# Kernel optimization log

Measured on AMD Instinct MI355X. Metric: run time of the kernel, lower is better.

## Reference

```python
import jax, jax.numpy as jnp
import numpy as np

D_MODEL = 1024
N_HEADS = 16
HEAD_DIM = D_MODEL // N_HEADS
D_FF = 4096
B, T = 2, 2048
LN_EPS = 1e-5


def setup_inputs() -> dict:
    key = jax.random.key(0)
    ks = jax.random.split(key, 12)
    s = 0.02
    return {
        "x": jax.random.normal(ks[0], (B, T, D_MODEL), jnp.float32),
        "ln1_g": jnp.ones((D_MODEL,), jnp.float32),
        "ln1_b": jnp.zeros((D_MODEL,), jnp.float32),
        "w_qkv": jax.random.normal(ks[1], (D_MODEL, 3 * D_MODEL), jnp.float32) * s,
        "b_qkv": jnp.zeros((3 * D_MODEL,), jnp.float32),
        "w_out": jax.random.normal(ks[2], (D_MODEL, D_MODEL), jnp.float32) * s,
        "b_out": jnp.zeros((D_MODEL,), jnp.float32),
        "ln2_g": jnp.ones((D_MODEL,), jnp.float32),
        "ln2_b": jnp.zeros((D_MODEL,), jnp.float32),
        "w_ff1": jax.random.normal(ks[3], (D_MODEL, D_FF), jnp.float32) * s,
        "b_ff1": jnp.zeros((D_FF,), jnp.float32),
        "w_ff2": jax.random.normal(ks[4], (D_FF, D_MODEL), jnp.float32) * s,
        "b_ff2": jnp.zeros((D_MODEL,), jnp.float32),
    }


def _layernorm(x, g, b):
    mu = jnp.mean(x, axis=-1, keepdims=True)
    var = jnp.mean(jnp.square(x - mu), axis=-1, keepdims=True)
    return (x - mu) * jax.lax.rsqrt(var + LN_EPS) * g + b


def _attention(h, w_qkv, b_qkv, w_out, b_out):
    Bx, Tx, C = h.shape
    qkv = h @ w_qkv + b_qkv  # [B,T,3C]
    q, k, v = jnp.split(qkv, 3, axis=-1)
    # [B,H,T,Dh]
    q = q.reshape(Bx, Tx, N_HEADS, HEAD_DIM).transpose(0, 2, 1, 3)
    k = k.reshape(Bx, Tx, N_HEADS, HEAD_DIM).transpose(0, 2, 1, 3)
    v = v.reshape(Bx, Tx, N_HEADS, HEAD_DIM).transpose(0, 2, 1, 3)
    scale = 1.0 / np.sqrt(HEAD_DIM).astype(np.float32)
    scores = jnp.einsum("bhqd,bhkd->bhqk", q, k) * scale
    causal = jnp.tril(jnp.ones((Tx, Tx), bool))
    scores = jnp.where(causal[None, None], scores, -jnp.inf)
    attn = jax.nn.softmax(scores, axis=-1)
    out = jnp.einsum("bhqk,bhkd->bhqd", attn, v)
    out = out.transpose(0, 2, 1, 3).reshape(Bx, Tx, C)
    return out @ w_out + b_out


def reference(x, ln1_g, ln1_b, w_qkv, b_qkv, w_out, b_out,
              ln2_g, ln2_b, w_ff1, b_ff1, w_ff2, b_ff2):
    h = _layernorm(x, ln1_g, ln1_b)
    x = x + _attention(h, w_qkv, b_qkv, w_out, b_out)
    h2 = _layernorm(x, ln2_g, ln2_b)
    ff = jax.nn.relu(h2 @ w_ff1 + b_ff1) @ w_ff2 + b_ff2
    return x + ff
```

## Files before the change

### kernel.cpp

```cpp
#include <hip/hip_runtime.h>


typedef unsigned short u16;
typedef __attribute__((ext_vector_type(8))) short     bf16x8;
typedef __attribute__((ext_vector_type(4))) float     f32x4;
typedef __attribute__((ext_vector_type(8))) unsigned short u16x8;
typedef __attribute__((ext_vector_type(4))) unsigned short u16x4;

__device__ __forceinline__ u16 f2bf(float f) {
    unsigned u = __builtin_bit_cast(unsigned, f);
    unsigned r = (u + 0x7fffu + ((u >> 16) & 1u)) >> 16;
    return (u16)r;
}
__device__ __forceinline__ float bf2f(u16 h) {
    unsigned u = ((unsigned)h) << 16;
    return __builtin_bit_cast(float, u);
}
__device__ __forceinline__ f32x4 mfma16(bf16x8 a, bf16x8 b, f32x4 c) {
    return __builtin_amdgcn_mfma_f32_16x16x32_bf16(a, b, c, 0, 0, 0);
}
__device__ __forceinline__ void gl_lds16(const u16* g, u16* l) {
    __builtin_amdgcn_global_load_lds((const __attribute__((address_space(1))) void*)g,
                                     (__attribute__((address_space(3))) void*)l, 16, 0, 0);
}

__global__ __launch_bounds__(256) void wconv_kernel(const float* __restrict__ in, u16* __restrict__ out,
                                                    int R, int C) {
    __shared__ float t[32][33];
    const int tx = threadIdx.x, ty = threadIdx.y;
    const int c0 = blockIdx.x * 32, r0 = blockIdx.y * 32;
#pragma unroll
    for (int i = 0; i < 4; ++i)
        t[ty + 8 * i][tx] = in[(size_t)(r0 + ty + 8 * i) * C + c0 + tx];
    __syncthreads();
#pragma unroll
    for (int i = 0; i < 4; ++i)
        out[(size_t)(c0 + ty + 8 * i) * R + r0 + tx] = f2bf(t[tx][ty + 8 * i]);
}

__global__ __launch_bounds__(256) void ln_kernel(const float* __restrict__ x, const float* __restrict__ g,
                                                 const float* __restrict__ b, u16* __restrict__ out) {
    const int row = blockIdx.x, tid = threadIdx.x;
    const float4 v = ((const float4*)(x + (size_t)row * 1024))[tid];
    float s = v.x + v.y + v.z + v.w;
    float q = v.x * v.x + v.y * v.y + v.z * v.z + v.w * v.w;
#pragma unroll
    for (int o = 32; o; o >>= 1) { s += __shfl_xor(s, o); q += __shfl_xor(q, o); }
    __shared__ float red[8];
    if ((tid & 63) == 0) { red[(tid >> 6) * 2] = s; red[(tid >> 6) * 2 + 1] = q; }
    __syncthreads();
    s = red[0] + red[2] + red[4] + red[6];
    q = red[1] + red[3] + red[5] + red[7];
    const float mu = s * (1.0f / 1024.0f);
    const float var = q * (1.0f / 1024.0f) - mu * mu;
    const float rs = rsqrtf(var + 1e-5f);
    const float4 gv = ((const float4*)g)[tid];
    const float4 bv = ((const float4*)b)[tid];
    u16x4 o;
    o[0] = f2bf((v.x - mu) * rs * gv.x + bv.x);
    o[1] = f2bf((v.y - mu) * rs * gv.y + bv.y);
    o[2] = f2bf((v.z - mu) * rs * gv.z + bv.z);
    o[3] = f2bf((v.w - mu) * rs * gv.w + bv.w);
    ((u16x4*)(out + (size_t)row * 1024))[tid] = o;
}

template <int MODE>
__global__ __launch_bounds__(256) void gemm_kernel(const u16* __restrict__ A, const u16* __restrict__ Bt,
                                                   const float* __restrict__ bias, const float* __restrict__ resid,
                                                   void* __restrict__ Cout, int M, int N, int K) {
    __shared__ __align__(16) u16 lds[2][2][4096];
    const int tid = threadIdx.x, lane = tid & 63, wid = tid >> 6;
    const int wr = wid >> 1, wc = wid & 1, lg = lane >> 4, lc = lane & 15;
    const int m0 = blockIdx.x * 128, n0 = blockIdx.y * 128;

    const u16* ga0 = A + (size_t)(m0 + (tid >> 2)) * K + (tid & 3) * 8;
    const u16* gb0 = Bt + (size_t)(n0 + (tid >> 2)) * K + (tid & 3) * 8;

    f32x4 acc[4][4];
#pragma unroll
    for (int m = 0; m < 4; ++m)
#pragma unroll
        for (int n = 0; n < 4; ++n) acc[m][n] = (f32x4){0.f, 0.f, 0.f, 0.f};

    const int NT = K >> 5;
    auto stage = [&](int buf, int kt) {
        const u16* ga = ga0 + kt * 32;
        const u16* gb = gb0 + kt * 32;
        gl_lds16(ga, &lds[buf][0][tid * 8]);
        gl_lds16(ga + (size_t)64 * K, &lds[buf][0][2048 + tid * 8]);
        gl_lds16(gb, &lds[buf][1][tid * 8]);
        gl_lds16(gb + (size_t)64 * K, &lds[buf][1][2048 + tid * 8]);
    };
    stage(0, 0);
    for (int kt = 0; kt < NT; ++kt) {
        __syncthreads();
        if (kt + 1 < NT) stage((kt + 1) & 1, kt + 1);
        const u16* la = &lds[kt & 1][0][0];
        const u16* lb = &lds[kt & 1][1][0];
        bf16x8 a[4], bb[4];
#pragma unroll
        for (int m = 0; m < 4; ++m) a[m] = *(const bf16x8*)(la + (wr * 64 + m * 16 + lc) * 32 + lg * 8);
#pragma unroll
        for (int n = 0; n < 4; ++n) bb[n] = *(const bf16x8*)(lb + (wc * 64 + n * 16 + lc) * 32 + lg * 8);
#pragma unroll
        for (int m = 0; m < 4; ++m)
#pragma unroll
            for (int n = 0; n < 4; ++n) acc[m][n] = mfma16(a[m], bb[n], acc[m][n]);
    }
#pragma unroll
    for (int m = 0; m < 4; ++m) {
        const int row = m0 + wr * 64 + m * 16 + lg * 4;
#pragma unroll
        for (int n = 0; n < 4; ++n) {
            const int col = n0 + wc * 64 + n * 16 + lc;
            const float bv = bias[col];
#pragma unroll
            for (int r = 0; r < 4; ++r) {
                float v = acc[m][n][r] + bv;
                if (MODE == 1) v = fmaxf(v, 0.0f);
                if (MODE == 2) {
                    v += resid[(size_t)(row + r) * N + col];
                    ((float*)Cout)[(size_t)(row + r) * N + col] = v;
                } else {
                    ((u16*)Cout)[(size_t)(row + r) * N + col] = f2bf(v);
                }
            }
        }
    }
}

__global__ __launch_bounds__(256) void vtrans_kernel(const u16* __restrict__ qkv, u16* __restrict__ v_t) {
    __shared__ u16 tile[64][72];
    const int bh = blockIdx.x >> 5, tt = blockIdx.x & 31;
    const int b = bh >> 4, h = bh & 15, t0 = tt * 64;
    const int tid = threadIdx.x;
    {
        const int tl = tid >> 2, seg = (tid & 3) * 16;
        const u16* src = qkv + (size_t)(b * 2048 + t0 + tl) * 3072 + 2048 + h * 64 + seg;
        u16x8 a = *(const u16x8*)src;
        u16x8 c = *(const u16x8*)(src + 8);
#pragma unroll
        for (int j = 0; j < 8; ++j) { tile[tl][seg + j] = a[j]; tile[tl][seg + 8 + j] = c[j]; }
    }
    __syncthreads();
    {
        const int d = tid >> 2, ts = (tid & 3) * 16;
        u16x8 o0, o1;
#pragma unroll
        for (int j = 0; j < 8; ++j) { o0[j] = tile[ts + j][d]; o1[j] = tile[ts + 8 + j][d]; }
        u16* dst = v_t + ((size_t)bh * 64 + d) * 2048 + t0 + ts;
        *(u16x8*)dst = o0;
        *(u16x8*)(dst + 8) = o1;
    }
}

__global__ __launch_bounds__(256) void attn_kernel(const u16* __restrict__ qkv, const u16* __restrict__ v_t,
                                                   u16* __restrict__ attnb) {
    __shared__ __align__(16) u16 wbuf[4][64 * 72];
    __shared__ float ml[4][2][64];
    const int tid = threadIdx.x, lane = tid & 63, wid = tid >> 6;
    const int lg = lane >> 4, lc = lane & 15;
    const int swz = (blockIdx.x & 7) * 128 + (blockIdx.x >> 3);
    const int qt = swz & 31, bh = swz >> 5;
    const int b = bh >> 4, h = bh & 15;
    const int q0 = qt * 64;
    u16* pl = &wbuf[wid][0];

    const u16* qbase = qkv + (size_t)b * 2048 * 3072 + h * 64;
    const u16* kbase = qbase + 1024;

    bf16x8 qf[2][4];
#pragma unroll
    for (int ks = 0; ks < 2; ++ks)
#pragma unroll
        for (int nf = 0; nf < 4; ++nf)
            qf[ks][nf] = *(const bf16x8*)(qbase + (size_t)(q0 + nf * 16 + lc) * 3072 + ks * 32 + lg * 8);

    f32x4 o[4][4];
#pragma unroll
    for (int i = 0; i < 4; ++i)
#pragma unroll
        for (int j = 0; j < 4; ++j) o[i][j] = (f32x4){0.f, 0.f, 0.f, 0.f};
    float mrow[4] = {-1e30f, -1e30f, -1e30f, -1e30f};
    float lrow[4] = {0.f, 0.f, 0.f, 0.f};

    const int nkt = 2 * qt + 2;
    for (int kt = wid; kt < nkt; kt += 4) {
        const int t0 = kt * 32;
        f32x4 s[2][4];
#pragma unroll
        for (int mf = 0; mf < 2; ++mf)
#pragma unroll
            for (int nf = 0; nf < 4; ++nf) s[mf][nf] = (f32x4){0.f, 0.f, 0.f, 0.f};
#pragma unroll
        for (int mf = 0; mf < 2; ++mf) {
            bf16x8 k0 = *(const bf16x8*)(kbase + (size_t)(t0 + mf * 16 + lc) * 3072 + lg * 8);
            bf16x8 k1 = *(const bf16x8*)(kbase + (size_t)(t0 + mf * 16 + lc) * 3072 + 32 + lg * 8);
#pragma unroll
            for (int nf = 0; nf < 4; ++nf) {
                s[mf][nf] = mfma16(k0, qf[0][nf], s[mf][nf]);
                s[mf][nf] = mfma16(k1, qf[1][nf], s[mf][nf]);
            }
        }
        const bool diag = (kt >= 2 * qt);
#pragma unroll
        for (int mf = 0; mf < 2; ++mf)
#pragma unroll
            for (int nf = 0; nf < 4; ++nf)
#pragma unroll
                for (int r = 0; r < 4; ++r) {
                    float v = s[mf][nf][r] * 0.125f;
                    if (diag) {
                        const int kv = t0 + mf * 16 + lg * 4 + r;
                        const int qq = q0 + nf * 16 + lc;
                        if (kv > qq) v = -1e30f;
                    }
                    s[mf][nf][r] = v;
                }
#pragma unroll
        for (int nf = 0; nf < 4; ++nf) {
            float cm = s[0][nf][0];
#pragma unroll
            for (int mf = 0; mf < 2; ++mf)
#pragma unroll
                for (int r = 0; r < 4; ++r) cm = fmaxf(cm, s[mf][nf][r]);
            cm = fmaxf(cm, __shfl_xor(cm, 16));
            cm = fmaxf(cm, __shfl_xor(cm, 32));
            const float mn = fmaxf(mrow[nf], cm);
            const float fac = __expf(mrow[nf] - mn);
            mrow[nf] = mn;
            float cs = 0.f;
#pragma unroll
            for (int mf = 0; mf < 2; ++mf)
#pragma unroll
                for (int r = 0; r < 4; ++r) {
                    const float p = __expf(s[mf][nf][r] - mn);
                    s[mf][nf][r] = p;
                    cs += p;
                }
            cs += __shfl_xor(cs, 16);
            cs += __shfl_xor(cs, 32);
            lrow[nf] = lrow[nf] * fac + cs;
#pragma unroll
            for (int mf2 = 0; mf2 < 4; ++mf2) o[mf2][nf] *= fac;
#pragma unroll
            for (int mf = 0; mf < 2; ++mf) {
                u16x4 pk;
                pk[0] = f2bf(s[mf][nf][0]);
                pk[1] = f2bf(s[mf][nf][1]);
                pk[2] = f2bf(s[mf][nf][2]);
                pk[3] = f2bf(s[mf][nf][3]);
                *(u16x4*)(pl + (nf * 16 + lc) * 40 + mf * 16 + lg * 4) = pk;
            }
        }
        bf16x8 pb[4];
#pragma unroll
        for (int nf = 0; nf < 4; ++nf)
            pb[nf] = *(const bf16x8*)(pl + (nf * 16 + lc) * 40 + lg * 8);
#pragma unroll
        for (int mf2 = 0; mf2 < 4; ++mf2) {
            bf16x8 vf = *(const bf16x8*)(v_t + ((size_t)bh * 64 + mf2 * 16 + lc) * 2048 + t0 + lg * 8);
#pragma unroll
            for (int nf = 0; nf < 4; ++nf) o[mf2][nf] = mfma16(vf, pb[nf], o[mf2][nf]);
        }
    }
    u16* po = &wbuf[wid][0];
#pragma unroll
    for (int mf2 = 0; mf2 < 4; ++mf2)
#pragma unroll
        for (int nf = 0; nf < 4; ++nf) {
            u16x4 pk;
            pk[0] = f2bf(o[mf2][nf][0]);
            pk[1] = f2bf(o[mf2][nf][1]);
            pk[2] = f2bf(o[mf2][nf][2]);
            pk[3] = f2bf(o[mf2][nf][3]);
            *(u16x4*)(po + (nf * 16 + lc) * 72 + mf2 * 16 + lg * 4) = pk;
        }
    if (lg == 0) {
#pragma unroll
        for (int nf = 0; nf < 4; ++nf) {
            ml[wid][0][nf * 16 + lc] = mrow[nf];
            ml[wid][1][nf * 16 + lc] = lrow[nf];
        }
    }
    __syncthreads();
#pragma unroll
    for (int rep = 0; rep < 2; ++rep) {
        const int it = tid + rep * 256;
        const int q = it >> 3, oc = it & 7;
        float mv[4], lv[4];
#pragma unroll
        for (int w = 0; w < 4; ++w) { mv[w] = ml[w][0][q]; lv[w] = ml[w][1][q]; }
        const float M = fmaxf(fmaxf(mv[0], mv[1]), fmaxf(mv[2], mv[3]));
        float fw[4], L = 0.f;
#pragma unroll
        for (int w = 0; w < 4; ++w) { fw[w] = __expf(mv[w] - M); L += lv[w] * fw[w]; }
        const float invL = 1.0f / L;
        float acc[8] = {0.f, 0.f, 0.f, 0.f, 0.f, 0.f, 0.f, 0.f};
#pragma unroll
        for (int w = 0; w < 4; ++w) {
            u16x8 v = *(const u16x8*)(&wbuf[w][q * 72 + oc * 8]);
#pragma unroll
            for (int j = 0; j < 8; ++j) acc[j] += bf2f(v[j]) * fw[w];
        }
        u16x8 ov;
#pragma unroll
        for (int j = 0; j < 8; ++j) ov[j] = f2bf(acc[j] * invL);
        *(u16x8*)(attnb + (size_t)(b * 2048 + q0 + q) * 1024 + h * 64 + oc * 8) = ov;
    }
}

extern "C" void kernel_launch(void* const* d_in, const int* in_sizes, int n_in,
                              void* d_out, int out_size, void* d_ws, size_t ws_size,
                              hipStream_t stream) {
    const float* x = (const float*)d_in[0];
    const float* ln1_g = (const float*)d_in[1];
    const float* ln1_b = (const float*)d_in[2];
    const float* w_qkv = (const float*)d_in[3];
    const float* b_qkv = (const float*)d_in[4];
    const float* w_out = (const float*)d_in[5];
    const float* b_out = (const float*)d_in[6];
    const float* ln2_g = (const float*)d_in[7];
    const float* ln2_b = (const float*)d_in[8];
    const float* w_ff1 = (const float*)d_in[9];
    const float* b_ff1 = (const float*)d_in[10];
    const float* w_ff2 = (const float*)d_in[11];
    const float* b_ff2 = (const float*)d_in[12];
    float* out = (float*)d_out;
    char* ws = (char*)d_ws;

    u16* wTqkv = (u16*)(ws + 0);
    u16* wTout = (u16*)(ws + 6291456);
    u16* wTff1 = (u16*)(ws + 8388608);
    u16* wTff2 = (u16*)(ws + 16777216);
    u16* h1    = (u16*)(ws + 25165824);
    u16* qkv   = (u16*)(ws + 33554432);
    u16* v_t   = (u16*)(ws + 58720256);
    u16* attnb = (u16*)(ws + 67108864);
    float* x2  = (float*)(ws + 75497472);
    u16* h2    = (u16*)(ws + 92274688);
    u16* ff1   = (u16*)(ws + 25165824);

    wconv_kernel<<<dim3(96, 32), dim3(32, 8), 0, stream>>>(w_qkv, wTqkv, 1024, 3072);
    wconv_kernel<<<dim3(32, 32), dim3(32, 8), 0, stream>>>(w_out, wTout, 1024, 1024);
    wconv_kernel<<<dim3(128, 32), dim3(32, 8), 0, stream>>>(w_ff1, wTff1, 1024, 4096);
    wconv_kernel<<<dim3(32, 128), dim3(32, 8), 0, stream>>>(w_ff2, wTff2, 4096, 1024);

    ln_kernel<<<4096, 256, 0, stream>>>(x, ln1_g, ln1_b, h1);
    gemm_kernel<0><<<dim3(32, 24), 256, 0, stream>>>(h1, wTqkv, b_qkv, nullptr, qkv, 4096, 3072, 1024);
    vtrans_kernel<<<1024, 256, 0, stream>>>(qkv, v_t);
    attn_kernel<<<1024, 256, 0, stream>>>(qkv, v_t, attnb);
    gemm_kernel<2><<<dim3(32, 8), 256, 0, stream>>>(attnb, wTout, b_out, x, x2, 4096, 1024, 1024);
    ln_kernel<<<4096, 256, 0, stream>>>(x2, ln2_g, ln2_b, h2);
    gemm_kernel<1><<<dim3(32, 32), 256, 0, stream>>>(h2, wTff1, b_ff1, nullptr, ff1, 4096, 4096, 1024);
    gemm_kernel<2><<<dim3(32, 8), 256, 0, stream>>>(ff1, wTff2, b_ff2, x2, out, 4096, 1024, 4096);
}
```

Measured before the change: 366.2 us.

## Pair causal attention query tiles per block and use narrower GEMM tiles for N=1024

The attention kernel now gives each block two query tiles, j and 31-j, processed one after the other, so every block does the same amount of causal work and half as many blocks are launched. The GEMM kernel gains a BN template parameter. The two N=1024 GEMMs (output projection and FF2) use 128x64 tiles, which doubles their grid from 256 to 512 blocks for better CU occupancy. In exchange, each attention block's two phases run serially and add extra barriers, and the narrower GEMM tiles reuse less data per block.

```diff
diff --git a/kernel.cpp b/kernel.cpp
--- a/kernel.cpp
+++ b/kernel.cpp
@@ -64,21 +64,24 @@
     ((u16x4*)(out + (size_t)row * 1024))[tid] = o;
 }
 
-template <int MODE>
+template <int MODE, int BN>
 __global__ __launch_bounds__(256) void gemm_kernel(const u16* __restrict__ A, const u16* __restrict__ Bt,
                                                    const float* __restrict__ bias, const float* __restrict__ resid,
                                                    void* __restrict__ Cout, int M, int N, int K) {
     __shared__ __align__(16) u16 lds[2][2][4096];
+    constexpr int MR = (BN == 128) ? 4 : 2;
     const int tid = threadIdx.x, lane = tid & 63, wid = tid >> 6;
-    const int wr = wid >> 1, wc = wid & 1, lg = lane >> 4, lc = lane & 15;
-    const int m0 = blockIdx.x * 128, n0 = blockIdx.y * 128;
+    const int wr = (BN == 128) ? (wid >> 1) : wid;
+    const int wc = (BN == 128) ? (wid & 1) : 0;
+    const int lg = lane >> 4, lc = lane & 15;
+    const int m0 = blockIdx.x * 128, n0 = blockIdx.y * BN;
 
     const u16* ga0 = A + (size_t)(m0 + (tid >> 2)) * K + (tid & 3) * 8;
     const u16* gb0 = Bt + (size_t)(n0 + (tid >> 2)) * K + (tid & 3) * 8;
 
-    f32x4 acc[4][4];
-#pragma unroll
-    for (int m = 0; m < 4; ++m)
+    f32x4 acc[MR][4];
+#pragma unroll
+    for (int m = 0; m < MR; ++m)
 #pragma unroll
         for (int n = 0; n < 4; ++n) acc[m][n] = (f32x4){0.f, 0.f, 0.f, 0.f};
 
@@ -89,7 +92,7 @@
         gl_lds16(ga, &lds[buf][0][tid * 8]);
         gl_lds16(ga + (size_t)64 * K, &lds[buf][0][2048 + tid * 8]);
         gl_lds16(gb, &lds[buf][1][tid * 8]);
-        gl_lds16(gb + (size_t)64 * K, &lds[buf][1][2048 + tid * 8]);
+        if (BN == 128) gl_lds16(gb + (size_t)64 * K, &lds[buf][1][2048 + tid * 8]);
     };
     stage(0, 0);
     for (int kt = 0; kt < NT; ++kt) {
@@ -97,19 +100,19 @@
         if (kt + 1 < NT) stage((kt + 1) & 1, kt + 1);
         const u16* la = &lds[kt & 1][0][0];
         const u16* lb = &lds[kt & 1][1][0];
-        bf16x8 a[4], bb[4];
-#pragma unroll
-        for (int m = 0; m < 4; ++m) a[m] = *(const bf16x8*)(la + (wr * 64 + m * 16 + lc) * 32 + lg * 8);
+        bf16x8 a[MR], bb[4];
+#pragma unroll
+        for (int m = 0; m < MR; ++m) a[m] = *(const bf16x8*)(la + (wr * (MR * 16) + m * 16 + lc) * 32 + lg * 8);
 #pragma unroll
         for (int n = 0; n < 4; ++n) bb[n] = *(const bf16x8*)(lb + (wc * 64 + n * 16 + lc) * 32 + lg * 8);
 #pragma unroll
-        for (int m = 0; m < 4; ++m)
+        for (int m = 0; m < MR; ++m)
 #pragma unroll
             for (int n = 0; n < 4; ++n) acc[m][n] = mfma16(a[m], bb[n], acc[m][n]);
     }
 #pragma unroll
-    for (int m = 0; m < 4; ++m) {
-        const int row = m0 + wr * 64 + m * 16 + lg * 4;
+    for (int m = 0; m < MR; ++m) {
+        const int row = m0 + wr * (MR * 16) + m * 16 + lg * 4;
 #pragma unroll
         for (int n = 0; n < 4; ++n) {
             const int col = n0 + wc * 64 + n * 16 + lc;
@@ -160,153 +163,158 @@
     __shared__ float ml[4][2][64];
     const int tid = threadIdx.x, lane = tid & 63, wid = tid >> 6;
     const int lg = lane >> 4, lc = lane & 15;
-    const int swz = (blockIdx.x & 7) * 128 + (blockIdx.x >> 3);
-    const int qt = swz & 31, bh = swz >> 5;
+    const int swz = (blockIdx.x & 7) * 64 + (blockIdx.x >> 3);
+    const int j = swz & 15, bh = swz >> 4;
     const int b = bh >> 4, h = bh & 15;
-    const int q0 = qt * 64;
     u16* pl = &wbuf[wid][0];
 
     const u16* qbase = qkv + (size_t)b * 2048 * 3072 + h * 64;
     const u16* kbase = qbase + 1024;
 
-    bf16x8 qf[2][4];
-#pragma unroll
-    for (int ks = 0; ks < 2; ++ks)
-#pragma unroll
-        for (int nf = 0; nf < 4; ++nf)
-            qf[ks][nf] = *(const bf16x8*)(qbase + (size_t)(q0 + nf * 16 + lc) * 3072 + ks * 32 + lg * 8);
-
-    f32x4 o[4][4];
-#pragma unroll
-    for (int i = 0; i < 4; ++i)
-#pragma unroll
-        for (int j = 0; j < 4; ++j) o[i][j] = (f32x4){0.f, 0.f, 0.f, 0.f};
-    float mrow[4] = {-1e30f, -1e30f, -1e30f, -1e30f};
-    float lrow[4] = {0.f, 0.f, 0.f, 0.f};
-
-    const int nkt = 2 * qt + 2;
-    for (int kt = wid; kt < nkt; kt += 4) {
-        const int t0 = kt * 32;
-        f32x4 s[2][4];
-#pragma unroll
-        for (int mf = 0; mf < 2; ++mf)
-#pragma unroll
-            for (int nf = 0; nf < 4; ++nf) s[mf][nf] = (f32x4){0.f, 0.f, 0.f, 0.f};
-#pragma unroll
-        for (int mf = 0; mf < 2; ++mf) {
-            bf16x8 k0 = *(const bf16x8*)(kbase + (size_t)(t0 + mf * 16 + lc) * 3072 + lg * 8);
-            bf16x8 k1 = *(const bf16x8*)(kbase + (size_t)(t0 + mf * 16 + lc) * 3072 + 32 + lg * 8);
+    for (int ph = 0; ph < 2; ++ph) {
+        const int qt = ph ? (31 - j) : j;
+        const int q0 = qt * 64;
+
+        bf16x8 qf[2][4];
+#pragma unroll
+        for (int ks = 0; ks < 2; ++ks)
+#pragma unroll
+            for (int nf = 0; nf < 4; ++nf)
+                qf[ks][nf] = *(const bf16x8*)(qbase + (size_t)(q0 + nf * 16 + lc) * 3072 + ks * 32 + lg * 8);
+
+        f32x4 o[4][4];
+#pragma unroll
+        for (int i = 0; i < 4; ++i)
+#pragma unroll
+            for (int jj = 0; jj < 4; ++jj) o[i][jj] = (f32x4){0.f, 0.f, 0.f, 0.f};
+        float mrow[4] = {-1e30f, -1e30f, -1e30f, -1e30f};
+        float lrow[4] = {0.f, 0.f, 0.f, 0.f};
+
+        const int nkt = 2 * qt + 2;
+        for (int kt = wid; kt < nkt; kt += 4) {
+            const int t0 = kt * 32;
+            f32x4 s[2][4];
+#pragma unroll
+            for (int mf = 0; mf < 2; ++mf)
+#pragma unroll
+                for (int nf = 0; nf < 4; ++nf) s[mf][nf] = (f32x4){0.f, 0.f, 0.f, 0.f};
+#pragma unroll
+            for (int mf = 0; mf < 2; ++mf) {
+                bf16x8 k0 = *(const bf16x8*)(kbase + (size_t)(t0 + mf * 16 + lc) * 3072 + lg * 8);
+                bf16x8 k1 = *(const bf16x8*)(kbase + (size_t)(t0 + mf * 16 + lc) * 3072 + 32 + lg * 8);
+#pragma unroll
+                for (int nf = 0; nf < 4; ++nf) {
+                    s[mf][nf] = mfma16(k0, qf[0][nf], s[mf][nf]);
+                    s[mf][nf] = mfma16(k1, qf[1][nf], s[mf][nf]);
+                }
+            }
+            const bool diag = (kt >= 2 * qt);
+#pragma unroll
+            for (int mf = 0; mf < 2; ++mf)
+#pragma unroll
+                for (int nf = 0; nf < 4; ++nf)
+#pragma unroll
+                    for (int r = 0; r < 4; ++r) {
+                        float v = s[mf][nf][r] * 0.125f;
+                        if (diag) {
+                            const int kv = t0 + mf * 16 + lg * 4 + r;
+                            const int qq = q0 + nf * 16 + lc;
+                            if (kv > qq) v = -1e30f;
+                        }
+                        s[mf][nf][r] = v;
+                    }
 #pragma unroll
             for (int nf = 0; nf < 4; ++nf) {
-                s[mf][nf] = mfma16(k0, qf[0][nf], s[mf][nf]);
-                s[mf][nf] = mfma16(k1, qf[1][nf], s[mf][nf]);
+                float cm = s[0][nf][0];
+#pragma unroll
+                for (int mf = 0; mf < 2; ++mf)
+#pragma unroll
+                    for (int r = 0; r < 4; ++r) cm = fmaxf(cm, s[mf][nf][r]);
+                cm = fmaxf(cm, __shfl_xor(cm, 16));
+                cm = fmaxf(cm, __shfl_xor(cm, 32));
+                const float mn = fmaxf(mrow[nf], cm);
+                const float fac = __expf(mrow[nf] - mn);
+                mrow[nf] = mn;
+                float cs = 0.f;
+#pragma unroll
+                for (int mf = 0; mf < 2; ++mf)
+#pragma unroll
+                    for (int r = 0; r < 4; ++r) {
+                        const float p = __expf(s[mf][nf][r] - mn);
+                        s[mf][nf][r] = p;
+                        cs += p;
+                    }
+                cs += __shfl_xor(cs, 16);
+                cs += __shfl_xor(cs, 32);
+                lrow[nf] = lrow[nf] * fac + cs;
+#pragma unroll
+                for (int mf2 = 0; mf2 < 4; ++mf2) o[mf2][nf] *= fac;
+#pragma unroll
+                for (int mf = 0; mf < 2; ++mf) {
+                    u16x4 pk;
+                    pk[0] = f2bf(s[mf][nf][0]);
+                    pk[1] = f2bf(s[mf][nf][1]);
+                    pk[2] = f2bf(s[mf][nf][2]);
+                    pk[3] = f2bf(s[mf][nf][3]);
+                    *(u16x4*)(pl + (nf * 16 + lc) * 40 + mf * 16 + lg * 4) = pk;
+                }
+            }
+            bf16x8 pb[4];
+#pragma unroll
+            for (int nf = 0; nf < 4; ++nf)
+                pb[nf] = *(const bf16x8*)(pl + (nf * 16 + lc) * 40 + lg * 8);
+#pragma unroll
+            for (int mf2 = 0; mf2 < 4; ++mf2) {
+                bf16x8 vf = *(const bf16x8*)(v_t + ((size_t)bh * 64 + mf2 * 16 + lc) * 2048 + t0 + lg * 8);
+#pragma unroll
+                for (int nf = 0; nf < 4; ++nf) o[mf2][nf] = mfma16(vf, pb[nf], o[mf2][nf]);
             }
         }
-        const bool diag = (kt >= 2 * qt);
-#pragma unroll
-        for (int mf = 0; mf < 2; ++mf)
-#pragma unroll
-            for (int nf = 0; nf < 4; ++nf)
-#pragma unroll
-                for (int r = 0; r < 4; ++r) {
-                    float v = s[mf][nf][r] * 0.125f;
-                    if (diag) {
-                        const int kv = t0 + mf * 16 + lg * 4 + r;
-                        const int qq = q0 + nf * 16 + lc;
-                        if (kv > qq) v = -1e30f;
-                    }
-                    s[mf][nf][r] = v;
-                }
-#pragma unroll
-        for (int nf = 0; nf < 4; ++nf) {
-            float cm = s[0][nf][0];
-#pragma unroll
-            for (int mf = 0; mf < 2; ++mf)
-#pragma unroll
-                for (int r = 0; r < 4; ++r) cm = fmaxf(cm, s[mf][nf][r]);
-            cm = fmaxf(cm, __shfl_xor(cm, 16));
-            cm = fmaxf(cm, __shfl_xor(cm, 32));
-            const float mn = fmaxf(mrow[nf], cm);
-            const float fac = __expf(mrow[nf] - mn);
-            mrow[nf] = mn;
-            float cs = 0.f;
-#pragma unroll
-            for (int mf = 0; mf < 2; ++mf)
-#pragma unroll
-                for (int r = 0; r < 4; ++r) {
-                    const float p = __expf(s[mf][nf][r] - mn);
-                    s[mf][nf][r] = p;
-                    cs += p;
-                }
-            cs += __shfl_xor(cs, 16);
-            cs += __shfl_xor(cs, 32);
-            lrow[nf] = lrow[nf] * fac + cs;
-#pragma unroll
-            for (int mf2 = 0; mf2 < 4; ++mf2) o[mf2][nf] *= fac;
-#pragma unroll
-            for (int mf = 0; mf < 2; ++mf) {
+        u16* po = &wbuf[wid][0];
+#pragma unroll
+        for (int mf2 = 0; mf2 < 4; ++mf2)
+#pragma unroll
+            for (int nf = 0; nf < 4; ++nf) {
                 u16x4 pk;
-                pk[0] = f2bf(s[mf][nf][0]);
-                pk[1] = f2bf(s[mf][nf][1]);
-                pk[2] = f2bf(s[mf][nf][2]);
-                pk[3] = f2bf(s[mf][nf][3]);
-                *(u16x4*)(pl + (nf * 16 + lc) * 40 + mf * 16 + lg * 4) = pk;
+                pk[0] = f2bf(o[mf2][nf][0]);
+                pk[1] = f2bf(o[mf2][nf][1]);
+                pk[2] = f2bf(o[mf2][nf][2]);
+                pk[3] = f2bf(o[mf2][nf][3]);
+                *(u16x4*)(po + (nf * 16 + lc) * 72 + mf2 * 16 + lg * 4) = pk;
+            }
+        if (lg == 0) {
+#pragma unroll
+            for (int nf = 0; nf < 4; ++nf) {
+                ml[wid][0][nf * 16 + lc] = mrow[nf];
+                ml[wid][1][nf * 16 + lc] = lrow[nf];
             }
         }
-        bf16x8 pb[4];
-#pragma unroll
-        for (int nf = 0; nf < 4; ++nf)
-            pb[nf] = *(const bf16x8*)(pl + (nf * 16 + lc) * 40 + lg * 8);
-#pragma unroll
-        for (int mf2 = 0; mf2 < 4; ++mf2) {
-            bf16x8 vf = *(const bf16x8*)(v_t + ((size_t)bh * 64 + mf2 * 16 + lc) * 2048 + t0 + lg * 8);
-#pragma unroll
-            for (int nf = 0; nf < 4; ++nf) o[mf2][nf] = mfma16(vf, pb[nf], o[mf2][nf]);
+        __syncthreads();
+#pragma unroll
+        for (int rep = 0; rep < 2; ++rep) {
+            const int it = tid + rep * 256;
+            const int q = it >> 3, oc = it & 7;
+            float mv[4], lv[4];
+#pragma unroll
+            for (int w = 0; w < 4; ++w) { mv[w] = ml[w][0][q]; lv[w] = ml[w][1][q]; }
+            const float M = fmaxf(fmaxf(mv[0], mv[1]), fmaxf(mv[2], mv[3]));
+            float fw[4], L = 0.f;
+#pragma unroll
+            for (int w = 0; w < 4; ++w) { fw[w] = __expf(mv[w] - M); L += lv[w] * fw[w]; }
+            const float invL = 1.0f / L;
+            float acc[8] = {0.f, 0.f, 0.f, 0.f, 0.f, 0.f, 0.f, 0.f};
+#pragma unroll
+            for (int w = 0; w < 4; ++w) {
+                u16x8 v = *(const u16x8*)(&wbuf[w][q * 72 + oc * 8]);
+#pragma unroll
+                for (int jj = 0; jj < 8; ++jj) acc[jj] += bf2f(v[jj]) * fw[w];
+            }
+            u16x8 ov;
+#pragma unroll
+            for (int jj = 0; jj < 8; ++jj) ov[jj] = f2bf(acc[jj] * invL);
+            *(u16x8*)(attnb + (size_t)(b * 2048 + q0 + q) * 1024 + h * 64 + oc * 8) = ov;
         }
-    }
-    u16* po = &wbuf[wid][0];
-#pragma unroll
-    for (int mf2 = 0; mf2 < 4; ++mf2)
-#pragma unroll
-        for (int nf = 0; nf < 4; ++nf) {
-            u16x4 pk;
-            pk[0] = f2bf(o[mf2][nf][0]);
-            pk[1] = f2bf(o[mf2][nf][1]);
-            pk[2] = f2bf(o[mf2][nf][2]);
-            pk[3] = f2bf(o[mf2][nf][3]);
-            *(u16x4*)(po + (nf * 16 + lc) * 72 + mf2 * 16 + lg * 4) = pk;
-        }
-    if (lg == 0) {
-#pragma unroll
-        for (int nf = 0; nf < 4; ++nf) {
-            ml[wid][0][nf * 16 + lc] = mrow[nf];
-            ml[wid][1][nf * 16 + lc] = lrow[nf];
-        }
-    }
-    __syncthreads();
-#pragma unroll
-    for (int rep = 0; rep < 2; ++rep) {
-        const int it = tid + rep * 256;
-        const int q = it >> 3, oc = it & 7;
-        float mv[4], lv[4];
-#pragma unroll
-        for (int w = 0; w < 4; ++w) { mv[w] = ml[w][0][q]; lv[w] = ml[w][1][q]; }
-        const float M = fmaxf(fmaxf(mv[0], mv[1]), fmaxf(mv[2], mv[3]));
-        float fw[4], L = 0.f;
-#pragma unroll
-        for (int w = 0; w < 4; ++w) { fw[w] = __expf(mv[w] - M); L += lv[w] * fw[w]; }
-        const float invL = 1.0f / L;
-        float acc[8] = {0.f, 0.f, 0.f, 0.f, 0.f, 0.f, 0.f, 0.f};
-#pragma unroll
-        for (int w = 0; w < 4; ++w) {
-            u16x8 v = *(const u16x8*)(&wbuf[w][q * 72 + oc * 8]);
-#pragma unroll
-            for (int j = 0; j < 8; ++j) acc[j] += bf2f(v[j]) * fw[w];
-        }
-        u16x8 ov;
-#pragma unroll
-        for (int j = 0; j < 8; ++j) ov[j] = f2bf(acc[j] * invL);
-        *(u16x8*)(attnb + (size_t)(b * 2048 + q0 + q) * 1024 + h * 64 + oc * 8) = ov;
+        __syncthreads();
     }
 }
 
@@ -347,11 +355,11 @@
     wconv_kernel<<<dim3(32, 128), dim3(32, 8), 0, stream>>>(w_ff2, wTff2, 4096, 1024);
 
     ln_kernel<<<4096, 256, 0, stream>>>(x, ln1_g, ln1_b, h1);
-    gemm_kernel<0><<<dim3(32, 24), 256, 0, stream>>>(h1, wTqkv, b_qkv, nullptr, qkv, 4096, 3072, 1024);
+    gemm_kernel<0, 128><<<dim3(32, 24), 256, 0, stream>>>(h1, wTqkv, b_qkv, nullptr, qkv, 4096, 3072, 1024);
     vtrans_kernel<<<1024, 256, 0, stream>>>(qkv, v_t);
-    attn_kernel<<<1024, 256, 0, stream>>>(qkv, v_t, attnb);
-    gemm_kernel<2><<<dim3(32, 8), 256, 0, stream>>>(attnb, wTout, b_out, x, x2, 4096, 1024, 1024);
+    attn_kernel<<<512, 256, 0, stream>>>(qkv, v_t, attnb);
+    gemm_kernel<2, 64><<<dim3(32, 16), 256, 0, stream>>>(attnb, wTout, b_out, x, x2, 4096, 1024, 1024);
     ln_kernel<<<4096, 256, 0, stream>>>(x2, ln2_g, ln2_b, h2);
-    gemm_kernel<1><<<dim3(32, 32), 256, 0, stream>>>(h2, wTff1, b_ff1, nullptr, ff1, 4096, 4096, 1024);
-    gemm_kernel<2><<<dim3(32, 8), 256, 0, stream>>>(ff1, wTff2, b_ff2, x2, out, 4096, 1024, 4096);
-}
+    gemm_kernel<1, 128><<<dim3(32, 32), 256, 0, stream>>>(h2, wTff1, b_ff1, nullptr, ff1, 4096, 4096, 1024);
+    gemm_kernel<2, 64><<<dim3(32, 16), 256, 0, stream>>>(ff1, wTff2, b_ff2, x2, out, 4096, 1024, 4096);
+}
```

New measurement: 382.7 us. 1.04x slower.
